# Optimization experiments

Measured on AMD Instinct MI355X. Metric: run time of the kernel, lower is better.

## Reference

```python
import jax, jax.numpy as jnp
import numpy as np

HID = 256   # hidden_dim
P = 16      # pool_size
EPS = 1e-5


def _ln(x, g, b):
    m = x.mean(-1, keepdims=True)
    v = x.var(-1, keepdims=True)
    return (x - m) * jax.lax.rsqrt(v + EPS) * g + b


def setup_inputs() -> dict:
    key = jax.random.key(0)
    ks = jax.random.split(key, 12)
    B, Cf, H, W = 8, 512, 64, 64
    Cg = Cf // 2
    Co = Cf // 2
    s = 0.02
    d = {}
    d['e_f'] = jax.random.normal(ks[0], (B, Cf, H, W), jnp.float32)
    d['e_g'] = jax.random.normal(ks[1], (B, Cg, H, W), jnp.float32)
    d['l_feat'] = jax.random.normal(ks[2], (B, 768, 20), jnp.float32)
    d['l_mask'] = jnp.ones((B, 20, 1), jnp.float32)
    d['ln_f_g'] = jnp.ones((Cf,), jnp.float32)
    d['ln_f_b'] = jnp.zeros((Cf,), jnp.float32)
    d['ln_g_g'] = jnp.ones((Cg,), jnp.float32)
    d['ln_g_b'] = jnp.zeros((Cg,), jnp.float32)
    d['wq'] = jax.random.normal(ks[3], (Cf, HID), jnp.float32) * s
    d['bq'] = jnp.zeros((HID,), jnp.float32)
    d['wk'] = jax.random.normal(ks[4], (Cg, HID), jnp.float32) * s
    d['bk'] = jnp.zeros((HID,), jnp.float32)
    d['wv'] = jax.random.normal(ks[5], (Cg, HID), jnp.float32) * s
    d['bv'] = jnp.zeros((HID,), jnp.float32)
    d['wo'] = jax.random.normal(ks[6], (HID, HID), jnp.float32) * s
    d['bo'] = jnp.zeros((HID,), jnp.float32)
    d['dw_k'] = jax.random.normal(ks[7], (HID, 1, 3, 3), jnp.float32) * s  # depthwise kernel (OIHW, I=1)
    d['efp_w'] = jax.random.normal(ks[8], (HID, Cf), jnp.float32) * s     # 1x1 conv v_channels->hidden
    d['efp_b'] = jnp.zeros((HID,), jnp.float32)
    d['outc_w'] = jax.random.normal(ks[9], (Co, HID), jnp.float32) * s    # 1x1 conv hidden->out
    d['outc_b'] = jnp.zeros((Co,), jnp.float32)
    d['bn_g'] = jnp.ones((Co,), jnp.float32)
    d['bn_b'] = jnp.zeros((Co,), jnp.float32)
    d['bn_m'] = jnp.zeros((Co,), jnp.float32)
    d['bn_v'] = jnp.ones((Co,), jnp.float32)
    return d


def reference(e_f, e_g, l_feat, l_mask, ln_f_g, ln_f_b, ln_g_g, ln_g_b,
              wq, bq, wk, bk, wv, bv, wo, bo, dw_k, efp_w, efp_b,
              outc_w, outc_b, bn_g, bn_b, bn_m, bn_v):
    B, Cf, H, W = e_f.shape
    # Q = w_qi(LN(e_f))                                  (B, HW, HID)
    q = _ln(e_f.transpose(0, 2, 3, 1), ln_f_g, ln_f_b).reshape(B, H * W, Cf) @ wq + bq
    # K/V projections from LN(e_g)
    g = _ln(e_g.transpose(0, 2, 3, 1), ln_g_g, ln_g_b).reshape(B, H * W, -1)
    k = (g @ wk + bk).reshape(B, H, W, HID)
    v = (g @ wv + bv).reshape(B, H, W, HID)
    # 16x16 max/avg pooling -> (B, Hp*Wp, HID)
    k = jnp.max(k.reshape(B, H // P, P, W // P, P, HID), axis=(2, 4)).reshape(B, -1, HID)
    v = jnp.mean(v.reshape(B, H // P, P, W // P, P, HID), axis=(2, 4)).reshape(B, -1, HID)
    # pooled attention
    attn = jax.nn.softmax(jnp.einsum('bqd,bkd->bqk', q, k) * (HID ** -0.5), axis=-1)
    a_i = jnp.einsum('bqk,bkd->bqd', attn, v)  # (B, HW, HID)
    # depthwise 3x3 conv on Q (NCHW)
    q_nchw = q.reshape(B, H, W, HID).transpose(0, 3, 1, 2)
    dw = jax.lax.conv_general_dilated(q_nchw, dw_k, (1, 1), [(1, 1), (1, 1)],
                                      feature_group_count=HID)
    combined = dw + a_i.reshape(B, H, W, HID).transpose(0, 3, 1, 2)
    comb = combined.transpose(0, 2, 3, 1).reshape(B, H * W, HID) @ wo + bo
    comb = comb.reshape(B, H, W, HID).transpose(0, 3, 1, 2)
    # 1x1 proj of e_f, elementwise gate
    efp = jnp.einsum('bchw,oc->bohw', e_f, efp_w) + efp_b[None, :, None, None]
    e_a = efp * comb
    # out: 1x1 conv + BN (inference) + ReLU (dropout inactive in eval)
    out = jnp.einsum('bchw,oc->bohw', e_a, outc_w) + outc_b[None, :, None, None]
    scale = (bn_g * jax.lax.rsqrt(bn_v + EPS))[None, :, None, None]
    out = (out - bn_m[None, :, None, None]) * scale + bn_b[None, :, None, None]
    return jax.nn.relu(out)
```

## Files before the change

### kernel.cpp

```cpp
#include <hip/hip_runtime.h>
#include <math.h>

#define EPS 1e-5f

typedef __attribute__((ext_vector_type(8))) short bf16x8;
typedef __attribute__((ext_vector_type(4))) float f32x4;

__device__ __forceinline__ unsigned short f2bf(float f) {
    unsigned int u = __float_as_uint(f);
    u += 0x7fff + ((u >> 16) & 1);
    return (unsigned short)(u >> 16);
}
__device__ __forceinline__ float bf2f(unsigned short h) {
    return __uint_as_float(((unsigned int)h) << 16);
}
__device__ __forceinline__ float lof(unsigned int u) {
    return __uint_as_float(u << 16);
}
__device__ __forceinline__ float hif(unsigned int u) {
    return __uint_as_float(u & 0xffff0000u);
}
__device__ __forceinline__ void async16(void* lds, const void* g) {
    __builtin_amdgcn_global_load_lds(
        (const __attribute__((address_space(1))) unsigned int*)g,
        (__attribute__((address_space(3))) unsigned int*)lds, 16, 0, 0);
}

__global__ __launch_bounds__(256) void prep_weights_bf(
    const float* __restrict__ lnfg, const float* __restrict__ wq,
    const float* __restrict__ efpw,
    const float* __restrict__ lngg, const float* __restrict__ wk,
    const float* __restrict__ wv, const float* __restrict__ wo,
    const float* __restrict__ outcw, const float* __restrict__ dwk,
    unsigned short* __restrict__ Wb1t, unsigned short* __restrict__ Wb2t,
    unsigned short* __restrict__ Wot, unsigned short* __restrict__ Woc,
    float* __restrict__ dwt)
{
    int idx = blockIdx.x * 256 + threadIdx.x;
    if (idx < 262144) {
        int n = idx >> 9, k = idx & 511;
        float v = (n < 256) ? lnfg[k] * wq[k * 256 + n]
                            : efpw[(size_t)(n - 256) * 512 + k];
        Wb1t[idx] = f2bf(v);
    } else if (idx < 393216) {
        int j = idx - 262144; int n = j >> 8, k = j & 255;
        float v = (n < 256) ? lngg[k] * wk[k * 256 + n]
                            : lngg[k] * wv[k * 256 + (n - 256)];
        Wb2t[j] = f2bf(v);
    } else if (idx < 458752) {
        int j = idx - 393216; int n = j >> 8, k = j & 255;
        Wot[j] = f2bf(wo[k * 256 + n]);
    } else if (idx < 524288) {
        int j = idx - 458752;
        Woc[j] = f2bf(outcw[j]);
    } else if (idx < 524288 + 2304) {
        int j = idx - 524288; int tap = j >> 8, ch = j & 255;
        dwt[j] = dwk[ch * 9 + tap];
    }
}

__global__ __launch_bounds__(256) void prep_cols(
    const float* __restrict__ lnfg, const float* __restrict__ lnfb,
    const float* __restrict__ wq, const float* __restrict__ bq,
    const float* __restrict__ efpb,
    const float* __restrict__ lngg, const float* __restrict__ lngb,
    const float* __restrict__ wk, const float* __restrict__ bk,
    const float* __restrict__ wv, const float* __restrict__ bv,
    const float* __restrict__ outcb, const float* __restrict__ bng,
    const float* __restrict__ bnb, const float* __restrict__ bnm,
    const float* __restrict__ bnv,
    float* __restrict__ cs1, float* __restrict__ cst1,
    float* __restrict__ cs2, float* __restrict__ cst2,
    float* __restrict__ scv, float* __restrict__ shv)
{
    int idx = blockIdx.x * 256 + threadIdx.x;
    if (idx < 256) {
        int n = idx; float cs = 0.f, ct = 0.f;
        for (int k = 0; k < 512; k++) {
            float w = wq[k * 256 + n];
            cs += lnfg[k] * w; ct += lnfb[k] * w;
        }
        cs1[n] = cs; cst1[n] = ct + bq[n];
    } else if (idx < 512) {
        cs1[idx] = 0.f; cst1[idx] = efpb[idx - 256];
    } else if (idx < 768) {
        int n = idx - 512; float cs = 0.f, ct = 0.f;
        for (int k = 0; k < 256; k++) {
            float w = wk[k * 256 + n];
            cs += lngg[k] * w; ct += lngb[k] * w;
        }
        cs2[n] = cs; cst2[n] = ct + bk[n];
    } else if (idx < 1024) {
        int n = idx - 768; float cs = 0.f, ct = 0.f;
        for (int k = 0; k < 256; k++) {
            float w = wv[k * 256 + n];
            cs += lngg[k] * w; ct += lngb[k] * w;
        }
        cs2[256 + n] = cs; cst2[256 + n] = ct + bv[n];
    } else if (idx < 1280) {
        int n = idx - 1024;
        float s = bng[n] * rsqrtf(bnv[n] + EPS);
        scv[n] = s;
        shv[n] = (outcb[n] - bnm[n]) * s + bnb[n];
    }
}

__global__ __launch_bounds__(256) void transpose_cvt_stats(
    const float* __restrict__ src, unsigned short* __restrict__ dst,
    float* __restrict__ sumb, float* __restrict__ ssb, int C)
{
    __shared__ float tile[64][65];
    __shared__ float psum[4][64], pss[4][64];
    int b = blockIdx.z, c0 = blockIdx.y * 64, p0 = blockIdx.x * 64;
    const float* s = src + ((size_t)b * C + c0) * 4096 + p0;
    int t = threadIdx.x;
    int lane = t & 63, grp = t >> 6;
#pragma unroll
    for (int i = 0; i < 16; i++) {
        int c = i * 4 + grp;
        tile[c][lane] = s[(size_t)c * 4096 + lane];
    }
    __syncthreads();
    unsigned short* d = dst + ((size_t)(b * 4096 + p0)) * C + c0;
#pragma unroll
    for (int i = 0; i < 16; i++) {
        int p = i * 4 + grp;
        d[(size_t)p * C + lane] = f2bf(tile[lane][p]);
    }
    float sm = 0.f, sq = 0.f;
#pragma unroll
    for (int j = 0; j < 16; j++) {
        float v = tile[grp * 16 + j][lane];
        sm += v; sq += v * v;
    }
    psum[grp][lane] = sm; pss[grp][lane] = sq;
    __syncthreads();
    if (t < 64) {
        float fs = psum[0][t] + psum[1][t] + psum[2][t] + psum[3][t];
        float fq = pss[0][t] + pss[1][t] + pss[2][t] + pss[3][t];
        atomicAdd(&sumb[b * 4096 + p0 + t], fs);
        atomicAdd(&ssb[b * 4096 + p0 + t], fq);
    }
}

__global__ __launch_bounds__(256) void ln_finalize(
    const float* __restrict__ sf, const float* __restrict__ ssf,
    const float* __restrict__ sg, const float* __restrict__ ssg,
    float* __restrict__ mf, float* __restrict__ rf,
    float* __restrict__ mg, float* __restrict__ rg)
{
    int gp = blockIdx.x * 256 + threadIdx.x;
    float m = sf[gp] * (1.f / 512.f);
    float v = ssf[gp] * (1.f / 512.f) - m * m;
    mf[gp] = m; rf[gp] = rsqrtf(v + EPS);
    m = sg[gp] * (1.f / 256.f);
    v = ssg[gp] * (1.f / 256.f) - m * m;
    mg[gp] = m; rg[gp] = rsqrtf(v + EPS);
}

template<int K>
__device__ __forceinline__ void mfma_core(
    const unsigned short* __restrict__ A, const unsigned short* __restrict__ Bt,
    int m0, int n0, unsigned short* As, unsigned short* Bs, f32x4 acc[4][4])
{
    const int tid = threadIdx.x;
    const int wave = tid >> 6, lane = tid & 63;
    const int wm = (wave & 1) * 64, wn = (wave >> 1) * 64;
#pragma unroll
    for (int i = 0; i < 4; i++)
#pragma unroll
        for (int j = 0; j < 4; j++) acc[i][j] = (f32x4){0.f, 0.f, 0.f, 0.f};

    const int srow = wave * 32 + (lane >> 3);
    const int sg = (lane & 7) ^ ((lane >> 3) & 7);
    const unsigned short* ga = A + (size_t)(m0 + srow) * K + sg * 8;
    const unsigned short* gb = Bt + (size_t)(n0 + srow) * K + sg * 8;

    for (int k0 = 0; k0 < K; k0 += 64) {
#pragma unroll
        for (int t = 0; t < 4; t++) {
            async16(As + (wave * 32 + t * 8) * 64, ga + (size_t)t * 8 * K + k0);
            async16(Bs + (wave * 32 + t * 8) * 64, gb + (size_t)t * 8 * K + k0);
        }
        __syncthreads();
#pragma unroll
        for (int ks = 0; ks < 2; ks++) {
            bf16x8 af[4], bfr[4];
            int kb = ks * 4 + (lane >> 4);
            int slot = (kb ^ (lane & 7)) * 8;
#pragma unroll
            for (int i = 0; i < 4; i++) {
                int m = wm + i * 16 + (lane & 15);
                af[i] = *(const bf16x8*)&As[m * 64 + slot];
                int n = wn + i * 16 + (lane & 15);
                bfr[i] = *(const bf16x8*)&Bs[n * 64 + slot];
            }
#pragma unroll
            for (int i = 0; i < 4; i++)
#pragma unroll
                for (int j = 0; j < 4; j++)
                    acc[i][j] = __builtin_amdgcn_mfma_f32_16x16x32_bf16(
                        af[i], bfr[j], acc[i][j], 0, 0, 0);
        }
        __syncthreads();
    }
}

__global__ __launch_bounds__(256) void gemm1_mfma(
    const unsigned short* __restrict__ ef_bf, const unsigned short* __restrict__ Wb1t,
    const float* __restrict__ cs1, const float* __restrict__ cst1,
    const float* __restrict__ mf, const float* __restrict__ rf,
    unsigned short* __restrict__ qbuf, unsigned short* __restrict__ efpbuf)
{
    __shared__ unsigned short As[8192], Bs[8192];
    f32x4 acc[4][4];
    int m0 = blockIdx.x * 128, n0 = blockIdx.y * 128;
    mfma_core<512>(ef_bf, Wb1t, m0, n0, As, Bs, acc);
    int lane = threadIdx.x & 63, wave = threadIdx.x >> 6;
    int wm = (wave & 1) * 64, wn = (wave >> 1) * 64;
    bool isq = (n0 < 256);
#pragma unroll
    for (int i = 0; i < 4; i++) {
#pragma unroll
        for (int r = 0; r < 4; r++) {
            int gm = m0 + wm + i * 16 + ((lane >> 4) * 4) + r;
            float mean = mf[gm], rs = rf[gm];
#pragma unroll
            for (int j = 0; j < 4; j++) {
                int n = n0 + wn + j * 16 + (lane & 15);
                float v = acc[i][j][r];
                if (isq) {
                    float o = rs * (v - mean * cs1[n]) + cst1[n];
                    qbuf[(size_t)gm * 256 + n] = f2bf(o);
                } else {
                    efpbuf[(size_t)gm * 256 + (n - 256)] = f2bf(v + cst1[n]);
                }
            }
        }
    }
}

__global__ __launch_bounds__(256) void gemm2_mfma(
    const unsigned short* __restrict__ eg_bf, const unsigned short* __restrict__ Wb2t,
    const float* __restrict__ cs2, const float* __restrict__ cst2,
    const float* __restrict__ mg, const float* __restrict__ rg,
    unsigned short* __restrict__ kfull, unsigned short* __restrict__ vfull)
{
    __shared__ unsigned short As[8192], Bs[8192];
    f32x4 acc[4][4];
    int m0 = blockIdx.x * 128, n0 = blockIdx.y * 128;
    mfma_core<256>(eg_bf, Wb2t, m0, n0, As, Bs, acc);
    int lane = threadIdx.x & 63, wave = threadIdx.x >> 6;
    int wm = (wave & 1) * 64, wn = (wave >> 1) * 64;
    unsigned short* dst = (n0 < 256) ? kfull : vfull;
    int nsub = (n0 < 256) ? 0 : 256;
#pragma unroll
    for (int i = 0; i < 4; i++) {
#pragma unroll
        for (int r = 0; r < 4; r++) {
            int gm = m0 + wm + i * 16 + ((lane >> 4) * 4) + r;
            float mean = mg[gm], rs = rg[gm];
#pragma unroll
            for (int j = 0; j < 4; j++) {
                int n = n0 + wn + j * 16 + (lane & 15);
                float o = rs * (acc[i][j][r] - mean * cs2[n]) + cst2[n];
                dst[(size_t)gm * 256 + (n - nsub)] = f2bf(o);
            }
        }
    }
}

__global__ __launch_bounds__(256) void gemm3_mfma(
    const unsigned short* __restrict__ comb, const unsigned short* __restrict__ Wot,
    const float* __restrict__ bo, const unsigned short* __restrict__ efp,
    unsigned short* __restrict__ ea)
{
    __shared__ unsigned short As[8192], Bs[8192];
    f32x4 acc[4][4];
    int m0 = blockIdx.x * 128, n0 = blockIdx.y * 128;
    mfma_core<256>(comb, Wot, m0, n0, As, Bs, acc);
    int lane = threadIdx.x & 63, wave = threadIdx.x >> 6;
    int wm = (wave & 1) * 64, wn = (wave >> 1) * 64;
#pragma unroll
    for (int i = 0; i < 4; i++) {
#pragma unroll
        for (int r = 0; r < 4; r++) {
            int gm = m0 + wm + i * 16 + ((lane >> 4) * 4) + r;
#pragma unroll
            for (int j = 0; j < 4; j++) {
                int n = n0 + wn + j * 16 + (lane & 15);
                float o = (acc[i][j][r] + bo[n]) * bf2f(efp[(size_t)gm * 256 + n]);
                ea[(size_t)gm * 256 + n] = f2bf(o);
            }
        }
    }
}

__global__ __launch_bounds__(256) void gemm4_mfma(
    const unsigned short* __restrict__ Woc, const unsigned short* __restrict__ ea,
    const float* __restrict__ scv, const float* __restrict__ shv,
    float* __restrict__ outp)
{
    __shared__ unsigned short As[8192], Bs[8192];
    f32x4 acc[4][4];
    int m0 = blockIdx.x * 128, n0 = blockIdx.y * 128;
    mfma_core<256>(Woc, ea, m0, n0, As, Bs, acc);
    int lane = threadIdx.x & 63, wave = threadIdx.x >> 6;
    int wm = (wave & 1) * 64, wn = (wave >> 1) * 64;
#pragma unroll
    for (int i = 0; i < 4; i++) {
#pragma unroll
        for (int r = 0; r < 4; r++) {
            int co = m0 + wm + i * 16 + ((lane >> 4) * 4) + r;
            float s = scv[co], hh = shv[co];
#pragma unroll
            for (int j = 0; j < 4; j++) {
                int p = n0 + wn + j * 16 + (lane & 15);
                float o = fmaxf(fmaf(acc[i][j][r], s, hh), 0.f);
                outp[((size_t)(p >> 12)) * 1048576 + (size_t)co * 4096 + (p & 4095)] = o;
            }
        }
    }
}

__global__ __launch_bounds__(256) void pool_fused(
    const unsigned short* __restrict__ kfull, const unsigned short* __restrict__ vfull,
    unsigned short* __restrict__ kpb, float* __restrict__ vp)
{
    __shared__ float kmax_s[8 * 256], vsum_s[8 * 256];
    int id = blockIdx.x;
    int b = id >> 4, cell = id & 15;
    int hp = cell >> 2, wp = cell & 3;
    int t = threadIdx.x;
    int g8 = t & 31, rr = t >> 5;
    float kmx[8], vsm[8];
#pragma unroll
    for (int j = 0; j < 8; j++) { kmx[j] = -3.402823466e38f; vsm[j] = 0.f; }
#pragma unroll
    for (int rsub = 0; rsub < 2; rsub++) {
        int r = rr * 2 + rsub;
        int prow = (hp * 16 + r) * 64 + wp * 16;
        for (int cl = 0; cl < 16; cl++) {
            size_t basei = ((size_t)(b * 4096 + prow + cl)) * 256 + g8 * 8;
            uint4 kv = *(const uint4*)(kfull + basei);
            uint4 vv = *(const uint4*)(vfull + basei);
            kmx[0] = fmaxf(kmx[0], lof(kv.x)); kmx[1] = fmaxf(kmx[1], hif(kv.x));
            kmx[2] = fmaxf(kmx[2], lof(kv.y)); kmx[3] = fmaxf(kmx[3], hif(kv.y));
            kmx[4] = fmaxf(kmx[4], lof(kv.z)); kmx[5] = fmaxf(kmx[5], hif(kv.z));
            kmx[6] = fmaxf(kmx[6], lof(kv.w)); kmx[7] = fmaxf(kmx[7], hif(kv.w));
            vsm[0] += lof(vv.x); vsm[1] += hif(vv.x);
            vsm[2] += lof(vv.y); vsm[3] += hif(vv.y);
            vsm[4] += lof(vv.z); vsm[5] += hif(vv.z);
            vsm[6] += lof(vv.w); vsm[7] += hif(vv.w);
        }
    }
#pragma unroll
    for (int j = 0; j < 8; j++) {
        kmax_s[rr * 256 + g8 * 8 + j] = kmx[j];
        vsum_s[rr * 256 + g8 * 8 + j] = vsm[j];
    }
    __syncthreads();
    int o = t;
    float m = kmax_s[o], s = vsum_s[o];
#pragma unroll
    for (int r2 = 1; r2 < 8; r2++) {
        m = fmaxf(m, kmax_s[r2 * 256 + o]);
        s += vsum_s[r2 * 256 + o];
    }
    kpb[(size_t)(b * 16 + cell) * 256 + o] = f2bf(m);
    vp [(size_t)(b * 16 + cell) * 256 + o] = s * (1.f / 256.f);
}

__global__ __launch_bounds__(256) void attn_w(
    const unsigned short* __restrict__ qbuf, const unsigned short* __restrict__ kpb,
    float* __restrict__ attns)
{
    int wave = threadIdx.x >> 6, lane = threadIdx.x & 63;
    int id = blockIdx.x;
    int b = id & 7, seg = id >> 3;
    int m0 = b * 4096 + seg * 64 + wave * 16;
    int fr = lane & 15, quad = lane >> 4;
    const unsigned short* qrow = qbuf + (size_t)(m0 + fr) * 256 + quad * 8;
    const unsigned short* krow = kpb + (size_t)(b * 16 + fr) * 256 + quad * 8;
    f32x4 sacc = {0.f, 0.f, 0.f, 0.f};
#pragma unroll
    for (int ks = 0; ks < 8; ks++) {
        bf16x8 af = *(const bf16x8*)(qrow + ks * 32);
        bf16x8 bf_ = *(const bf16x8*)(krow + ks * 32);
        sacc = __builtin_amdgcn_mfma_f32_16x16x32_bf16(af, bf_, sacc, 0, 0, 0);
    }
#pragma unroll
    for (int r = 0; r < 4; r++) {
        float s = sacc[r] * 0.0625f;
        float mx = s;
#pragma unroll
        for (int off = 8; off >= 1; off >>= 1) mx = fmaxf(mx, __shfl_xor(mx, off));
        float e = __expf(s - mx);
        float sum = e;
#pragma unroll
        for (int off = 8; off >= 1; off >>= 1) sum += __shfl_xor(sum, off);
        attns[(size_t)(m0 + quad * 4 + r) * 16 + fr] = e / sum;
    }
}

__global__ __launch_bounds__(256) void combined_dw(
    const unsigned short* __restrict__ qbuf, const float* __restrict__ attns,
    const float* __restrict__ vp, const float* __restrict__ dwt,
    unsigned short* __restrict__ combined)
{
    int wave = threadIdx.x >> 6, lane = threadIdx.x & 63;
    int id = blockIdx.x;
    int b = id & 7, seg = id >> 3;
    int pidx = seg * 16 + wave * 4;
    int h = pidx >> 6, w0 = pidx & 63;
    int o4 = lane * 4;

    float4 kreg[9];
#pragma unroll
    for (int tap = 0; tap < 9; tap++)
        kreg[tap] = *(const float4*)&dwt[tap * 256 + o4];

    float4 acc[4];
#pragma unroll
    for (int i = 0; i < 4; i++) acc[i] = (float4){0.f, 0.f, 0.f, 0.f};

    const float* arow = attns + (size_t)(b * 4096 + pidx) * 16;
#pragma unroll
    for (int c = 0; c < 16; c++) {
        float4 v = *(const float4*)&vp[(size_t)(b * 16 + c) * 256 + o4];
#pragma unroll
        for (int i = 0; i < 4; i++) {
            float a = arow[i * 16 + c];
            acc[i].x = fmaf(a, v.x, acc[i].x); acc[i].y = fmaf(a, v.y, acc[i].y);
            acc[i].z = fmaf(a, v.z, acc[i].z); acc[i].w = fmaf(a, v.w, acc[i].w);
        }
    }
#pragma unroll
    for (int dy = 0; dy < 3; dy++) {
        int hh = h + dy - 1;
        if (hh < 0 || hh > 63) continue;
        const unsigned short* qr = qbuf + ((size_t)(b * 4096 + hh * 64)) * 256;
        float4 ft[6];
#pragma unroll
        for (int c = 0; c < 6; c++) {
            int xx = w0 - 1 + c;
            if (xx < 0 || xx > 63) {
                ft[c] = (float4){0.f, 0.f, 0.f, 0.f};
            } else {
                uint2 qa = *(const uint2*)(qr + (size_t)xx * 256 + o4);
                ft[c] = (float4){lof(qa.x), hif(qa.x), lof(qa.y), hif(qa.y)};
            }
        }
#pragma unroll
        for (int dx = 0; dx < 3; dx++) {
            float4 kk = kreg[dy * 3 + dx];
#pragma unroll
            for (int i = 0; i < 4; i++) {
                float4 qv = ft[i + dx];
                acc[i].x = fmaf(qv.x, kk.x, acc[i].x);
                acc[i].y = fmaf(qv.y, kk.y, acc[i].y);
                acc[i].z = fmaf(qv.z, kk.z, acc[i].z);
                acc[i].w = fmaf(qv.w, kk.w, acc[i].w);
            }
        }
    }
#pragma unroll
    for (int i = 0; i < 4; i++) {
        uint2 pk;
        pk.x = (unsigned)f2bf(acc[i].x) | ((unsigned)f2bf(acc[i].y) << 16);
        pk.y = (unsigned)f2bf(acc[i].z) | ((unsigned)f2bf(acc[i].w) << 16);
        *(uint2*)(combined + ((size_t)(b * 4096 + pidx + i)) * 256 + o4) = pk;
    }
}

extern "C" void kernel_launch(void* const* d_in, const int* in_sizes, int n_in,
                              void* d_out, int out_size, void* d_ws, size_t ws_size,
                              hipStream_t stream)
{
    const float* e_f   = (const float*)d_in[0];
    const float* e_g   = (const float*)d_in[1];
    const float* lnfg  = (const float*)d_in[4];
    const float* lnfb  = (const float*)d_in[5];
    const float* lngg  = (const float*)d_in[6];
    const float* lngb  = (const float*)d_in[7];
    const float* wq    = (const float*)d_in[8];
    const float* bq    = (const float*)d_in[9];
    const float* wk    = (const float*)d_in[10];
    const float* bk    = (const float*)d_in[11];
    const float* wv    = (const float*)d_in[12];
    const float* bv    = (const float*)d_in[13];
    const float* wo    = (const float*)d_in[14];
    const float* bo    = (const float*)d_in[15];
    const float* dwk   = (const float*)d_in[16];
    const float* efpw  = (const float*)d_in[17];
    const float* efpb  = (const float*)d_in[18];
    const float* outcw = (const float*)d_in[19];
    const float* outcb = (const float*)d_in[20];
    const float* bng   = (const float*)d_in[21];
    const float* bnb   = (const float*)d_in[22];
    const float* bnm   = (const float*)d_in[23];
    const float* bnv   = (const float*)d_in[24];
    float* outp = (float*)d_out;

    char* base = (char*)d_ws;
    auto alloc = [&](size_t bytes) -> char* {
        char* r = base; base += (bytes + 255) & ~(size_t)255; return r;
    };
    float* sumf = (float*)alloc(4 * 32768 * 4);
    float* ssf  = sumf + 32768;
    float* sumg = sumf + 65536;
    float* ssg  = sumf + 98304;
    float* mf    = (float*)alloc(32768 * 4);
    float* rf    = (float*)alloc(32768 * 4);
    float* mg    = (float*)alloc(32768 * 4);
    float* rg    = (float*)alloc(32768 * 4);
    float* cs1   = (float*)alloc(512 * 4);
    float* cst1  = (float*)alloc(512 * 4);
    float* cs2   = (float*)alloc(512 * 4);
    float* cst2  = (float*)alloc(512 * 4);
    float* scv   = (float*)alloc(256 * 4);
    float* shv   = (float*)alloc(256 * 4);
    float* dwt   = (float*)alloc(9 * 256 * 4);
    unsigned short* Wb1t = (unsigned short*)alloc(262144 * 2);
    unsigned short* Wb2t = (unsigned short*)alloc(131072 * 2);
    unsigned short* Wot  = (unsigned short*)alloc(65536 * 2);
    unsigned short* Woc  = (unsigned short*)alloc(65536 * 2);
    unsigned short* ef_bf = (unsigned short*)alloc((size_t)32768 * 512 * 2);
    unsigned short* eg_bf = (unsigned short*)alloc((size_t)32768 * 256 * 2);
    unsigned short* qbuf  = (unsigned short*)alloc((size_t)32768 * 256 * 2);
    unsigned short* efpbuf = (unsigned short*)alloc((size_t)32768 * 256 * 2);
    unsigned short* kfull = (unsigned short*)alloc((size_t)32768 * 256 * 2);
    unsigned short* vfull = (unsigned short*)alloc((size_t)32768 * 256 * 2);
    unsigned short* kpb  = (unsigned short*)alloc(128 * 256 * 2);
    float* vp    = (float*)alloc(128 * 256 * 4);
    float* attns = (float*)alloc((size_t)32768 * 16 * 4);

    hipMemsetAsync(sumf, 0, 4 * 32768 * 4, stream);
    prep_weights_bf<<<2057, 256, 0, stream>>>(lnfg, wq, efpw, lngg, wk, wv, wo,
                                              outcw, dwk, Wb1t, Wb2t, Wot, Woc, dwt);
    prep_cols<<<5, 256, 0, stream>>>(lnfg, lnfb, wq, bq, efpb,
                                     lngg, lngb, wk, bk, wv, bv,
                                     outcb, bng, bnb, bnm, bnv,
                                     cs1, cst1, cs2, cst2, scv, shv);
    transpose_cvt_stats<<<dim3(64, 8, 8), 256, 0, stream>>>(e_f, ef_bf, sumf, ssf, 512);
    transpose_cvt_stats<<<dim3(64, 4, 8), 256, 0, stream>>>(e_g, eg_bf, sumg, ssg, 256);
    ln_finalize<<<128, 256, 0, stream>>>(sumf, ssf, sumg, ssg, mf, rf, mg, rg);
    gemm1_mfma<<<dim3(256, 4), 256, 0, stream>>>(ef_bf, Wb1t, cs1, cst1, mf, rf,
                                                 qbuf, efpbuf);
    gemm2_mfma<<<dim3(256, 4), 256, 0, stream>>>(eg_bf, Wb2t, cs2, cst2, mg, rg,
                                                 kfull, vfull);
    pool_fused<<<128, 256, 0, stream>>>(kfull, vfull, kpb, vp);
    attn_w<<<512, 256, 0, stream>>>(qbuf, kpb, attns);
    combined_dw<<<2048, 256, 0, stream>>>(qbuf, attns, vp, dwt, kfull);
    gemm3_mfma<<<dim3(256, 2), 256, 0, stream>>>(kfull, Wot, bo,
                                                 efpbuf, vfull);
    gemm4_mfma<<<dim3(2, 256), 256, 0, stream>>>(Woc, vfull, scv, shv, outp);
}
```

Baseline: 347.9 us.

## Pool V before projection, fuse attention into dw kernel, merge prep and transposes

V is now computed by pooling the rstd-weighted e_g per cell and then projecting the pooled sums (linearity of LayerNorm plus projection plus mean). This drops the full V half of gemm2 and the vfull write and read. The attention softmax is fused into combined_dw through shared memory, so the attns buffer round trip goes away. The two prep kernels and the two transposes are each merged into one launch, and LN stats now use per-block partial writes instead of atomics, which removes the memset. In exchange, pool_phase reads e_g in fp32 again, and V gains precision because the pooled path stays in fp32.

New measurement: 340.0 us. -2.3%, faster.

```diff
diff --git a/kernel.cpp b/kernel.cpp
--- a/kernel.cpp
+++ b/kernel.cpp
@@ -26,15 +26,23 @@
         (__attribute__((address_space(3))) unsigned int*)lds, 16, 0, 0);
 }
 
-__global__ __launch_bounds__(256) void prep_weights_bf(
-    const float* __restrict__ lnfg, const float* __restrict__ wq,
-    const float* __restrict__ efpw,
-    const float* __restrict__ lngg, const float* __restrict__ wk,
-    const float* __restrict__ wv, const float* __restrict__ wo,
-    const float* __restrict__ outcw, const float* __restrict__ dwk,
+__global__ __launch_bounds__(256) void prep_all(
+    const float* __restrict__ lnfg, const float* __restrict__ lnfb,
+    const float* __restrict__ wq, const float* __restrict__ bq,
+    const float* __restrict__ efpw, const float* __restrict__ efpb,
+    const float* __restrict__ lngg, const float* __restrict__ lngb,
+    const float* __restrict__ wk, const float* __restrict__ bk,
+    const float* __restrict__ wv, const float* __restrict__ bv,
+    const float* __restrict__ wo, const float* __restrict__ outcw,
+    const float* __restrict__ outcb, const float* __restrict__ bng,
+    const float* __restrict__ bnb, const float* __restrict__ bnm,
+    const float* __restrict__ bnv, const float* __restrict__ dwk,
     unsigned short* __restrict__ Wb1t, unsigned short* __restrict__ Wb2t,
     unsigned short* __restrict__ Wot, unsigned short* __restrict__ Woc,
-    float* __restrict__ dwt)
+    float* __restrict__ dwt,
+    float* __restrict__ cs1, float* __restrict__ cst1,
+    float* __restrict__ cs2, float* __restrict__ cst2,
+    float* __restrict__ scv, float* __restrict__ shv)
 {
     int idx = blockIdx.x * 256 + threadIdx.x;
     if (idx < 262144) {
@@ -42,76 +50,72 @@
         float v = (n < 256) ? lnfg[k] * wq[k * 256 + n]
                             : efpw[(size_t)(n - 256) * 512 + k];
         Wb1t[idx] = f2bf(v);
+    } else if (idx < 327680) {
+        int j = idx - 262144; int n = j >> 8, k = j & 255;
+        Wb2t[j] = f2bf(lngg[k] * wk[k * 256 + n]);
     } else if (idx < 393216) {
-        int j = idx - 262144; int n = j >> 8, k = j & 255;
-        float v = (n < 256) ? lngg[k] * wk[k * 256 + n]
-                            : lngg[k] * wv[k * 256 + (n - 256)];
-        Wb2t[j] = f2bf(v);
+        int j = idx - 327680; int n = j >> 8, k = j & 255;
+        Wot[j] = f2bf(wo[k * 256 + n]);
     } else if (idx < 458752) {
-        int j = idx - 393216; int n = j >> 8, k = j & 255;
-        Wot[j] = f2bf(wo[k * 256 + n]);
-    } else if (idx < 524288) {
-        int j = idx - 458752;
+        int j = idx - 393216;
         Woc[j] = f2bf(outcw[j]);
-    } else if (idx < 524288 + 2304) {
-        int j = idx - 524288; int tap = j >> 8, ch = j & 255;
+    } else if (idx < 461056) {
+        int j = idx - 458752; int tap = j >> 8, ch = j & 255;
         dwt[j] = dwk[ch * 9 + tap];
-    }
-}
-
-__global__ __launch_bounds__(256) void prep_cols(
-    const float* __restrict__ lnfg, const float* __restrict__ lnfb,
-    const float* __restrict__ wq, const float* __restrict__ bq,
-    const float* __restrict__ efpb,
-    const float* __restrict__ lngg, const float* __restrict__ lngb,
-    const float* __restrict__ wk, const float* __restrict__ bk,
-    const float* __restrict__ wv, const float* __restrict__ bv,
-    const float* __restrict__ outcb, const float* __restrict__ bng,
-    const float* __restrict__ bnb, const float* __restrict__ bnm,
-    const float* __restrict__ bnv,
-    float* __restrict__ cs1, float* __restrict__ cst1,
-    float* __restrict__ cs2, float* __restrict__ cst2,
-    float* __restrict__ scv, float* __restrict__ shv)
-{
-    int idx = blockIdx.x * 256 + threadIdx.x;
-    if (idx < 256) {
-        int n = idx; float cs = 0.f, ct = 0.f;
-        for (int k = 0; k < 512; k++) {
-            float w = wq[k * 256 + n];
-            cs += lnfg[k] * w; ct += lnfb[k] * w;
-        }
-        cs1[n] = cs; cst1[n] = ct + bq[n];
-    } else if (idx < 512) {
-        cs1[idx] = 0.f; cst1[idx] = efpb[idx - 256];
-    } else if (idx < 768) {
-        int n = idx - 512; float cs = 0.f, ct = 0.f;
-        for (int k = 0; k < 256; k++) {
-            float w = wk[k * 256 + n];
-            cs += lngg[k] * w; ct += lngb[k] * w;
-        }
-        cs2[n] = cs; cst2[n] = ct + bk[n];
-    } else if (idx < 1024) {
-        int n = idx - 768; float cs = 0.f, ct = 0.f;
-        for (int k = 0; k < 256; k++) {
-            float w = wv[k * 256 + n];
-            cs += lngg[k] * w; ct += lngb[k] * w;
-        }
-        cs2[256 + n] = cs; cst2[256 + n] = ct + bv[n];
-    } else if (idx < 1280) {
-        int n = idx - 1024;
-        float s = bng[n] * rsqrtf(bnv[n] + EPS);
-        scv[n] = s;
-        shv[n] = (outcb[n] - bnm[n]) * s + bnb[n];
-    }
-}
-
-__global__ __launch_bounds__(256) void transpose_cvt_stats(
-    const float* __restrict__ src, unsigned short* __restrict__ dst,
-    float* __restrict__ sumb, float* __restrict__ ssb, int C)
+    } else if (idx < 462336) {
+        int j = idx - 461056;
+        if (j < 256) {
+            int n = j; float cs = 0.f, ct = 0.f;
+            for (int k = 0; k < 512; k++) {
+                float w = wq[k * 256 + n];
+                cs += lnfg[k] * w; ct += lnfb[k] * w;
+            }
+            cs1[n] = cs; cst1[n] = ct + bq[n];
+        } else if (j < 512) {
+            cs1[j] = 0.f; cst1[j] = efpb[j - 256];
+        } else if (j < 768) {
+            int n = j - 512; float cs = 0.f, ct = 0.f;
+            for (int k = 0; k < 256; k++) {
+                float w = wk[k * 256 + n];
+                cs += lngg[k] * w; ct += lngb[k] * w;
+            }
+            cs2[n] = cs; cst2[n] = ct + bk[n];
+        } else if (j < 1024) {
+            int n = j - 768; float cs = 0.f, ct = 0.f;
+            for (int k = 0; k < 256; k++) {
+                float w = wv[k * 256 + n];
+                cs += lngg[k] * w; ct += lngb[k] * w;
+            }
+            cs2[256 + n] = cs; cst2[256 + n] = ct + bv[n];
+        } else {
+            int n = j - 1024;
+            float s = bng[n] * rsqrtf(bnv[n] + EPS);
+            scv[n] = s;
+            shv[n] = (outcb[n] - bnm[n]) * s + bnb[n];
+        }
+    }
+}
+
+__global__ __launch_bounds__(256) void transpose_fg(
+    const float* __restrict__ ef, const float* __restrict__ eg,
+    unsigned short* __restrict__ ef_bf, unsigned short* __restrict__ eg_bf,
+    float* __restrict__ pf, float* __restrict__ pfq,
+    float* __restrict__ pg, float* __restrict__ pgq)
 {
     __shared__ float tile[64][65];
     __shared__ float psum[4][64], pss[4][64];
-    int b = blockIdx.z, c0 = blockIdx.y * 64, p0 = blockIdx.x * 64;
+    int id = blockIdx.x;
+    const float* src; unsigned short* dst; float* ps; float* pq;
+    int C, cblk, b, p0;
+    if (id < 4096) {
+        src = ef; dst = ef_bf; ps = pf; pq = pfq; C = 512;
+        p0 = (id & 63) * 64; cblk = (id >> 6) & 7; b = id >> 9;
+    } else {
+        id -= 4096;
+        src = eg; dst = eg_bf; ps = pg; pq = pgq; C = 256;
+        p0 = (id & 63) * 64; cblk = (id >> 6) & 3; b = id >> 8;
+    }
+    int c0 = cblk * 64;
     const float* s = src + ((size_t)b * C + c0) * 4096 + p0;
     int t = threadIdx.x;
     int lane = t & 63, grp = t >> 6;
@@ -138,23 +142,29 @@
     if (t < 64) {
         float fs = psum[0][t] + psum[1][t] + psum[2][t] + psum[3][t];
         float fq = pss[0][t] + pss[1][t] + pss[2][t] + pss[3][t];
-        atomicAdd(&sumb[b * 4096 + p0 + t], fs);
-        atomicAdd(&ssb[b * 4096 + p0 + t], fq);
+        ps[cblk * 32768 + b * 4096 + p0 + t] = fs;
+        pq[cblk * 32768 + b * 4096 + p0 + t] = fq;
     }
 }
 
 __global__ __launch_bounds__(256) void ln_finalize(
-    const float* __restrict__ sf, const float* __restrict__ ssf,
-    const float* __restrict__ sg, const float* __restrict__ ssg,
+    const float* __restrict__ pf, const float* __restrict__ pfq,
+    const float* __restrict__ pg, const float* __restrict__ pgq,
     float* __restrict__ mf, float* __restrict__ rf,
     float* __restrict__ mg, float* __restrict__ rg)
 {
     int gp = blockIdx.x * 256 + threadIdx.x;
-    float m = sf[gp] * (1.f / 512.f);
-    float v = ssf[gp] * (1.f / 512.f) - m * m;
+    float s = 0.f, q = 0.f;
+#pragma unroll
+    for (int i = 0; i < 8; i++) { s += pf[i * 32768 + gp]; q += pfq[i * 32768 + gp]; }
+    float m = s * (1.f / 512.f);
+    float v = q * (1.f / 512.f) - m * m;
     mf[gp] = m; rf[gp] = rsqrtf(v + EPS);
-    m = sg[gp] * (1.f / 256.f);
-    v = ssg[gp] * (1.f / 256.f) - m * m;
+    s = 0.f; q = 0.f;
+#pragma unroll
+    for (int i = 0; i < 4; i++) { s += pg[i * 32768 + gp]; q += pgq[i * 32768 + gp]; }
+    m = s * (1.f / 256.f);
+    v = q * (1.f / 256.f) - m * m;
     mg[gp] = m; rg[gp] = rsqrtf(v + EPS);
 }
 
@@ -240,11 +250,11 @@
     }
 }
 
-__global__ __launch_bounds__(256) void gemm2_mfma(
+__global__ __launch_bounds__(256) void gemm2k_mfma(
     const unsigned short* __restrict__ eg_bf, const unsigned short* __restrict__ Wb2t,
     const float* __restrict__ cs2, const float* __restrict__ cst2,
     const float* __restrict__ mg, const float* __restrict__ rg,
-    unsigned short* __restrict__ kfull, unsigned short* __restrict__ vfull)
+    unsigned short* __restrict__ kfull)
 {
     __shared__ unsigned short As[8192], Bs[8192];
     f32x4 acc[4][4];
@@ -252,8 +262,6 @@
     mfma_core<256>(eg_bf, Wb2t, m0, n0, As, Bs, acc);
     int lane = threadIdx.x & 63, wave = threadIdx.x >> 6;
     int wm = (wave & 1) * 64, wn = (wave >> 1) * 64;
-    unsigned short* dst = (n0 < 256) ? kfull : vfull;
-    int nsub = (n0 < 256) ? 0 : 256;
 #pragma unroll
     for (int i = 0; i < 4; i++) {
 #pragma unroll
@@ -264,7 +272,7 @@
             for (int j = 0; j < 4; j++) {
                 int n = n0 + wn + j * 16 + (lane & 15);
                 float o = rs * (acc[i][j][r] - mean * cs2[n]) + cst2[n];
-                dst[(size_t)gm * 256 + (n - nsub)] = f2bf(o);
+                kfull[(size_t)gm * 256 + n] = f2bf(o);
             }
         }
     }
@@ -323,95 +331,138 @@
     }
 }
 
-__global__ __launch_bounds__(256) void pool_fused(
-    const unsigned short* __restrict__ kfull, const unsigned short* __restrict__ vfull,
-    unsigned short* __restrict__ kpb, float* __restrict__ vp)
-{
-    __shared__ float kmax_s[8 * 256], vsum_s[8 * 256];
+__global__ __launch_bounds__(256) void pool_phase(
+    const unsigned short* __restrict__ kfull, const float* __restrict__ eg,
+    const float* __restrict__ rg, const float* __restrict__ mg,
+    unsigned short* __restrict__ kpb, float* __restrict__ s1,
+    float* __restrict__ s0)
+{
+    __shared__ float smem[4352];
     int id = blockIdx.x;
-    int b = id >> 4, cell = id & 15;
-    int hp = cell >> 2, wp = cell & 3;
     int t = threadIdx.x;
-    int g8 = t & 31, rr = t >> 5;
-    float kmx[8], vsm[8];
-#pragma unroll
-    for (int j = 0; j < 8; j++) { kmx[j] = -3.402823466e38f; vsm[j] = 0.f; }
-#pragma unroll
-    for (int rsub = 0; rsub < 2; rsub++) {
-        int r = rr * 2 + rsub;
-        int prow = (hp * 16 + r) * 64 + wp * 16;
-        for (int cl = 0; cl < 16; cl++) {
-            size_t basei = ((size_t)(b * 4096 + prow + cl)) * 256 + g8 * 8;
-            uint4 kv = *(const uint4*)(kfull + basei);
-            uint4 vv = *(const uint4*)(vfull + basei);
-            kmx[0] = fmaxf(kmx[0], lof(kv.x)); kmx[1] = fmaxf(kmx[1], hif(kv.x));
-            kmx[2] = fmaxf(kmx[2], lof(kv.y)); kmx[3] = fmaxf(kmx[3], hif(kv.y));
-            kmx[4] = fmaxf(kmx[4], lof(kv.z)); kmx[5] = fmaxf(kmx[5], hif(kv.z));
-            kmx[6] = fmaxf(kmx[6], lof(kv.w)); kmx[7] = fmaxf(kmx[7], hif(kv.w));
-            vsm[0] += lof(vv.x); vsm[1] += hif(vv.x);
-            vsm[2] += lof(vv.y); vsm[3] += hif(vv.y);
-            vsm[4] += lof(vv.z); vsm[5] += hif(vv.z);
-            vsm[6] += lof(vv.w); vsm[7] += hif(vv.w);
-        }
-    }
-#pragma unroll
-    for (int j = 0; j < 8; j++) {
-        kmax_s[rr * 256 + g8 * 8 + j] = kmx[j];
-        vsum_s[rr * 256 + g8 * 8 + j] = vsm[j];
-    }
-    __syncthreads();
-    int o = t;
-    float m = kmax_s[o], s = vsum_s[o];
-#pragma unroll
-    for (int r2 = 1; r2 < 8; r2++) {
-        m = fmaxf(m, kmax_s[r2 * 256 + o]);
-        s += vsum_s[r2 * 256 + o];
-    }
-    kpb[(size_t)(b * 16 + cell) * 256 + o] = f2bf(m);
-    vp [(size_t)(b * 16 + cell) * 256 + o] = s * (1.f / 256.f);
-}
-
-__global__ __launch_bounds__(256) void attn_w(
+    if (id < 128) {
+        int b = id >> 4, cell = id & 15;
+        int hp = cell >> 2, wp = cell & 3;
+        int g8 = t & 31, rr = t >> 5;
+        float kmx[8];
+#pragma unroll
+        for (int j = 0; j < 8; j++) kmx[j] = -3.402823466e38f;
+#pragma unroll
+        for (int rsub = 0; rsub < 2; rsub++) {
+            int r = rr * 2 + rsub;
+            int prow = (hp * 16 + r) * 64 + wp * 16;
+            for (int cl = 0; cl < 16; cl++) {
+                size_t basei = ((size_t)(b * 4096 + prow + cl)) * 256 + g8 * 8;
+                uint4 kv = *(const uint4*)(kfull + basei);
+                kmx[0] = fmaxf(kmx[0], lof(kv.x)); kmx[1] = fmaxf(kmx[1], hif(kv.x));
+                kmx[2] = fmaxf(kmx[2], lof(kv.y)); kmx[3] = fmaxf(kmx[3], hif(kv.y));
+                kmx[4] = fmaxf(kmx[4], lof(kv.z)); kmx[5] = fmaxf(kmx[5], hif(kv.z));
+                kmx[6] = fmaxf(kmx[6], lof(kv.w)); kmx[7] = fmaxf(kmx[7], hif(kv.w));
+            }
+        }
+#pragma unroll
+        for (int j = 0; j < 8; j++) smem[rr * 256 + g8 * 8 + j] = kmx[j];
+        __syncthreads();
+        float m = smem[t];
+#pragma unroll
+        for (int r2 = 1; r2 < 8; r2++) m = fmaxf(m, smem[r2 * 256 + t]);
+        kpb[(size_t)(b * 16 + cell) * 256 + t] = f2bf(m);
+    } else {
+        int id2 = id - 128;
+        int b = id2 >> 6, hp = (id2 >> 4) & 3, cgrp = id2 & 15;
+        int rr = t >> 4, cq = t & 15, cx = cq >> 2;
+        int p = (hp * 16 + rr) * 64 + cq * 4;
+        float4 w4 = *(const float4*)&rg[b * 4096 + p];
+        float part[16];
+        const float* egb = eg + ((size_t)b * 256 + cgrp * 16) * 4096 + p;
+#pragma unroll
+        for (int cc = 0; cc < 16; cc++) {
+            float4 v4 = *(const float4*)(egb + (size_t)cc * 4096);
+            part[cc] = w4.x * v4.x + w4.y * v4.y + w4.z * v4.z + w4.w * v4.w;
+        }
+#pragma unroll
+        for (int cc = 0; cc < 16; cc++) smem[t * 16 + cc] = part[cc];
+        if (cgrp == 0) {
+            float4 m4 = *(const float4*)&mg[b * 4096 + p];
+            smem[4096 + t] = w4.x * m4.x + w4.y * m4.y + w4.z * m4.z + w4.w * m4.w;
+        }
+        __syncthreads();
+        if (t < 64) {
+            int cx2 = t >> 4, cc = t & 15;
+            float sacc = 0.f;
+#pragma unroll
+            for (int rr2 = 0; rr2 < 16; rr2++)
+#pragma unroll
+                for (int dq = 0; dq < 4; dq++)
+                    sacc += smem[(rr2 * 16 + cx2 * 4 + dq) * 16 + cc];
+            s1[((size_t)(b * 16 + hp * 4 + cx2)) * 256 + cgrp * 16 + cc] = sacc;
+        }
+        if (cgrp == 0 && t < 4) {
+            float sacc = 0.f;
+#pragma unroll
+            for (int rr2 = 0; rr2 < 16; rr2++)
+#pragma unroll
+                for (int dq = 0; dq < 4; dq++)
+                    sacc += smem[4096 + rr2 * 16 + t * 4 + dq];
+            s0[b * 16 + hp * 4 + t] = sacc;
+        }
+    }
+}
+
+__global__ __launch_bounds__(256) void vpool_gemm(
+    const float* __restrict__ s1, const float* __restrict__ s0,
+    const float* __restrict__ lngg, const float* __restrict__ wv,
+    const float* __restrict__ cs2, const float* __restrict__ cst2,
+    float* __restrict__ vp)
+{
+    int cell = blockIdx.x;
+    int n = threadIdx.x;
+    const float* s1r = s1 + (size_t)cell * 256;
+    float acc = 0.f;
+    for (int c = 0; c < 256; c++)
+        acc = fmaf(lngg[c] * s1r[c], wv[c * 256 + n], acc);
+    vp[(size_t)cell * 256 + n] = acc * (1.f / 256.f)
+        - (s0[cell] * (1.f / 256.f)) * cs2[256 + n] + cst2[256 + n];
+}
+
+__global__ __launch_bounds__(256) void combined_dw(
     const unsigned short* __restrict__ qbuf, const unsigned short* __restrict__ kpb,
-    float* __restrict__ attns)
-{
+    const float* __restrict__ vp, const float* __restrict__ dwt,
+    unsigned short* __restrict__ combined)
+{
+    __shared__ float attns[256];
     int wave = threadIdx.x >> 6, lane = threadIdx.x & 63;
     int id = blockIdx.x;
     int b = id & 7, seg = id >> 3;
-    int m0 = b * 4096 + seg * 64 + wave * 16;
-    int fr = lane & 15, quad = lane >> 4;
-    const unsigned short* qrow = qbuf + (size_t)(m0 + fr) * 256 + quad * 8;
-    const unsigned short* krow = kpb + (size_t)(b * 16 + fr) * 256 + quad * 8;
-    f32x4 sacc = {0.f, 0.f, 0.f, 0.f};
-#pragma unroll
-    for (int ks = 0; ks < 8; ks++) {
-        bf16x8 af = *(const bf16x8*)(qrow + ks * 32);
-        bf16x8 bf_ = *(const bf16x8*)(krow + ks * 32);
-        sacc = __builtin_amdgcn_mfma_f32_16x16x32_bf16(af, bf_, sacc, 0, 0, 0);
-    }
-#pragma unroll
-    for (int r = 0; r < 4; r++) {
-        float s = sacc[r] * 0.0625f;
-        float mx = s;
-#pragma unroll
-        for (int off = 8; off >= 1; off >>= 1) mx = fmaxf(mx, __shfl_xor(mx, off));
-        float e = __expf(s - mx);
-        float sum = e;
-#pragma unroll
-        for (int off = 8; off >= 1; off >>= 1) sum += __shfl_xor(sum, off);
-        attns[(size_t)(m0 + quad * 4 + r) * 16 + fr] = e / sum;
-    }
-}
-
-__global__ __launch_bounds__(256) void combined_dw(
-    const unsigned short* __restrict__ qbuf, const float* __restrict__ attns,
-    const float* __restrict__ vp, const float* __restrict__ dwt,
-    unsigned short* __restrict__ combined)
-{
-    int wave = threadIdx.x >> 6, lane = threadIdx.x & 63;
-    int id = blockIdx.x;
-    int b = id & 7, seg = id >> 3;
-    int pidx = seg * 16 + wave * 4;
+    int pidx0 = seg * 16;
+
+    if (wave == 0) {
+        int fr = lane & 15, quad = lane >> 4;
+        const unsigned short* qrow = qbuf + (size_t)(b * 4096 + pidx0 + fr) * 256 + quad * 8;
+        const unsigned short* krow = kpb + (size_t)(b * 16 + fr) * 256 + quad * 8;
+        f32x4 sacc = {0.f, 0.f, 0.f, 0.f};
+#pragma unroll
+        for (int ks = 0; ks < 8; ks++) {
+            bf16x8 af = *(const bf16x8*)(qrow + ks * 32);
+            bf16x8 bf_ = *(const bf16x8*)(krow + ks * 32);
+            sacc = __builtin_amdgcn_mfma_f32_16x16x32_bf16(af, bf_, sacc, 0, 0, 0);
+        }
+#pragma unroll
+        for (int r = 0; r < 4; r++) {
+            float s = sacc[r] * 0.0625f;
+            float mx = s;
+#pragma unroll
+            for (int off = 8; off >= 1; off >>= 1) mx = fmaxf(mx, __shfl_xor(mx, off));
+            float e = __expf(s - mx);
+            float sum = e;
+#pragma unroll
+            for (int off = 8; off >= 1; off >>= 1) sum += __shfl_xor(sum, off);
+            attns[(quad * 4 + r) * 16 + fr] = e / sum;
+        }
+    }
+    __syncthreads();
+
+    int pidx = pidx0 + wave * 4;
     int h = pidx >> 6, w0 = pidx & 63;
     int o4 = lane * 4;
 
@@ -424,7 +475,7 @@
 #pragma unroll
     for (int i = 0; i < 4; i++) acc[i] = (float4){0.f, 0.f, 0.f, 0.f};
 
-    const float* arow = attns + (size_t)(b * 4096 + pidx) * 16;
+    const float* arow = attns + (wave * 4) * 16;
 #pragma unroll
     for (int c = 0; c < 16; c++) {
         float4 v = *(const float4*)&vp[(size_t)(b * 16 + c) * 256 + o4];
@@ -506,10 +557,10 @@
     auto alloc = [&](size_t bytes) -> char* {
         char* r = base; base += (bytes + 255) & ~(size_t)255; return r;
     };
-    float* sumf = (float*)alloc(4 * 32768 * 4);
-    float* ssf  = sumf + 32768;
-    float* sumg = sumf + 65536;
-    float* ssg  = sumf + 98304;
+    float* pf    = (float*)alloc(8 * 32768 * 4);
+    float* pfq   = (float*)alloc(8 * 32768 * 4);
+    float* pg    = (float*)alloc(4 * 32768 * 4);
+    float* pgq   = (float*)alloc(4 * 32768 * 4);
     float* mf    = (float*)alloc(32768 * 4);
     float* rf    = (float*)alloc(32768 * 4);
     float* mg    = (float*)alloc(32768 * 4);
@@ -522,7 +573,7 @@
     float* shv   = (float*)alloc(256 * 4);
     float* dwt   = (float*)alloc(9 * 256 * 4);
     unsigned short* Wb1t = (unsigned short*)alloc(262144 * 2);
-    unsigned short* Wb2t = (unsigned short*)alloc(131072 * 2);
+    unsigned short* Wb2t = (unsigned short*)alloc(65536 * 2);
     unsigned short* Wot  = (unsigned short*)alloc(65536 * 2);
     unsigned short* Woc  = (unsigned short*)alloc(65536 * 2);
     unsigned short* ef_bf = (unsigned short*)alloc((size_t)32768 * 512 * 2);
@@ -530,29 +581,27 @@
     unsigned short* qbuf  = (unsigned short*)alloc((size_t)32768 * 256 * 2);
     unsigned short* efpbuf = (unsigned short*)alloc((size_t)32768 * 256 * 2);
     unsigned short* kfull = (unsigned short*)alloc((size_t)32768 * 256 * 2);
-    unsigned short* vfull = (unsigned short*)alloc((size_t)32768 * 256 * 2);
+    unsigned short* ea    = (unsigned short*)alloc((size_t)32768 * 256 * 2);
     unsigned short* kpb  = (unsigned short*)alloc(128 * 256 * 2);
     float* vp    = (float*)alloc(128 * 256 * 4);
-    float* attns = (float*)alloc((size_t)32768 * 16 * 4);
-
-    hipMemsetAsync(sumf, 0, 4 * 32768 * 4, stream);
-    prep_weights_bf<<<2057, 256, 0, stream>>>(lnfg, wq, efpw, lngg, wk, wv, wo,
-                                              outcw, dwk, Wb1t, Wb2t, Wot, Woc, dwt);
-    prep_cols<<<5, 256, 0, stream>>>(lnfg, lnfb, wq, bq, efpb,
-                                     lngg, lngb, wk, bk, wv, bv,
-                                     outcb, bng, bnb, bnm, bnv,
-                                     cs1, cst1, cs2, cst2, scv, shv);
-    transpose_cvt_stats<<<dim3(64, 8, 8), 256, 0, stream>>>(e_f, ef_bf, sumf, ssf, 512);
-    transpose_cvt_stats<<<dim3(64, 4, 8), 256, 0, stream>>>(e_g, eg_bf, sumg, ssg, 256);
-    ln_finalize<<<128, 256, 0, stream>>>(sumf, ssf, sumg, ssg, mf, rf, mg, rg);
+    float* s1    = (float*)alloc(128 * 256 * 4);
+    float* s0    = (float*)alloc(128 * 4);
+
+    prep_all<<<1806, 256, 0, stream>>>(
+        lnfg, lnfb, wq, bq, efpw, efpb, lngg, lngb, wk, bk, wv, bv, wo,
+        outcw, outcb, bng, bnb, bnm, bnv, dwk,
+        Wb1t, Wb2t, Wot, Woc, dwt, cs1, cst1, cs2, cst2, scv, shv);
+    transpose_fg<<<6144, 256, 0, stream>>>(e_f, e_g, ef_bf, eg_bf,
+                                           pf, pfq, pg, pgq);
+    ln_finalize<<<128, 256, 0, stream>>>(pf, pfq, pg, pgq, mf, rf, mg, rg);
     gemm1_mfma<<<dim3(256, 4), 256, 0, stream>>>(ef_bf, Wb1t, cs1, cst1, mf, rf,
                                                  qbuf, efpbuf);
-    gemm2_mfma<<<dim3(256, 4), 256, 0, stream>>>(eg_bf, Wb2t, cs2, cst2, mg, rg,
-                                                 kfull, vfull);
-    pool_fused<<<128, 256, 0, stream>>>(kfull, vfull, kpb, vp);
-    attn_w<<<512, 256, 0, stream>>>(qbuf, kpb, attns);
-    combined_dw<<<2048, 256, 0, stream>>>(qbuf, attns, vp, dwt, kfull);
+    gemm2k_mfma<<<dim3(256, 2), 256, 0, stream>>>(eg_bf, Wb2t, cs2, cst2, mg, rg,
+                                                  kfull);
+    pool_phase<<<640, 256, 0, stream>>>(kfull, e_g, rg, mg, kpb, s1, s0);
+    vpool_gemm<<<128, 256, 0, stream>>>(s1, s0, lngg, wv, cs2, cst2, vp);
+    combined_dw<<<2048, 256, 0, stream>>>(qbuf, kpb, vp, dwt, kfull);
     gemm3_mfma<<<dim3(256, 2), 256, 0, stream>>>(kfull, Wot, bo,
-                                                 efpbuf, vfull);
-    gemm4_mfma<<<dim3(2, 256), 256, 0, stream>>>(Woc, vfull, scv, shv, outp);
-}
+                                                 efpbuf, ea);
+    gemm4_mfma<<<dim3(2, 256), 256, 0, stream>>>(Woc, ea, scv, shv, outp);
+}
```
